# Kernel optimization log

Hardware: AMD Instinct MI355X
Metric: run time of the kernel (lower is better)

## Reference

```python
import jax, jax.numpy as jnp
import numpy as np

N_HEADS = 16
COS_SIM_SCALE = 8.0  # lucidrains flash_cosine_sim_attention default temperature
RMS_EPS = 1e-6
ROPE_THETA = 10000.0


def _rms_norm(t, g):
    # RMSNorm over head dim with learnable gain (QKNorm)
    return t * jax.lax.rsqrt(jnp.mean(t * t, axis=-1, keepdims=True) + RMS_EPS) * g


def _rotate_half(x):
    d = x.shape[-1]
    return jnp.concatenate([-x[..., d // 2:], x[..., : d // 2]], axis=-1)


def _image_rope_cos_sin(n, d, dtype):
    # 2D axial RoPE: first half of head dim encodes row position, second half column.
    side = int(np.sqrt(n))
    assert side * side == n, 'ImageRoPE expects a square token grid'
    n_freq = d // 4
    freqs = 1.0 / (ROPE_THETA ** (jnp.arange(n_freq, dtype=jnp.float32) / n_freq))
    pos = jnp.arange(side, dtype=jnp.float32)
    grid_h = jnp.repeat(pos, side)   # (n,) row index
    grid_w = jnp.tile(pos, side)     # (n,) col index
    ang_h = grid_h[:, None] * freqs  # (n, d//4)
    ang_w = grid_w[:, None] * freqs  # (n, d//4)
    # rotate-half convention: angles for dims [0:d//2] paired with [d//2:d]
    ang = jnp.concatenate([ang_h, ang_w], axis=-1)          # (n, d//2)
    ang = jnp.concatenate([ang, ang], axis=-1)              # (n, d)
    return jnp.cos(ang).astype(dtype), jnp.sin(ang).astype(dtype)


def setup_inputs() -> dict:
    key = jax.random.key(0)
    ks = jax.random.split(key, 6)
    b, n, dm = 8, 1024, 1024
    h = N_HEADS
    d = dm // h
    s = 1.0 / np.sqrt(dm)
    return {
        'x': jax.random.normal(ks[0], (b, n, dm), dtype=jnp.float32),
        'w_qkv': jax.random.normal(ks[1], (dm, 3 * dm), dtype=jnp.float32) * s,
        'b_qkv': jnp.zeros((3 * dm,), dtype=jnp.float32),
        'q_gain': jnp.ones((d,), dtype=jnp.float32),
        'k_gain': jnp.ones((d,), dtype=jnp.float32),
        'w_out': jax.random.normal(ks[2], (dm, dm), dtype=jnp.float32) * s,
        'b_out': jnp.zeros((dm,), dtype=jnp.float32),
    }


def reference(x, w_qkv, b_qkv, q_gain, k_gain, w_out, b_out):
    b, n, dm = x.shape
    h = N_HEADS
    d = dm // h
    qkv = x @ w_qkv + b_qkv                       # (b, n, 3*dm)
    qkv = qkv.reshape(b, n, 3, h, d)
    qkv = jnp.transpose(qkv, (2, 0, 3, 1, 4))     # (3, b, h, n, d)
    q, k, v = qkv[0], qkv[1], qkv[2]
    # QK-norm (RMSNorm over head dim)
    q = _rms_norm(q, q_gain)
    k = _rms_norm(k, k_gain)
    # 2D image RoPE
    cos, sin = _image_rope_cos_sin(n, d, x.dtype)
    q = q * cos + _rotate_half(q) * sin
    k = k * cos + _rotate_half(k) * sin
    # cosine-sim attention: l2-normalize q,k, fixed scale, softmax, weighted sum
    q = q / jnp.linalg.norm(q, axis=-1, keepdims=True)
    k = k / jnp.linalg.norm(k, axis=-1, keepdims=True)
    scores = jnp.einsum('bhnd,bhmd->bhnm', q, k) * COS_SIM_SCALE
    attn = jax.nn.softmax(scores, axis=-1)
    o = jnp.einsum('bhnm,bhmd->bhnd', attn, v)    # (b, h, n, d)
    o = jnp.transpose(o, (0, 2, 1, 3)).reshape(b, n, dm)
    return o @ w_out + b_out
```

## Files before the change

kernel.cpp:

```cpp
#include <hip/hip_runtime.h>
#include <hip/hip_bf16.h>
#include <cstdint>

typedef __bf16 bf16;
typedef __bf16 bf16x8 __attribute__((ext_vector_type(8)));
typedef __bf16 bf16x4 __attribute__((ext_vector_type(4)));
typedef float f32x4 __attribute__((ext_vector_type(4)));

__device__ inline bf16x8 cvt8(const float* __restrict__ p) {
  float4 a = *(const float4*)p;
  float4 b = *(const float4*)(p + 4);
  bf16x8 r;
  r[0] = (bf16)a.x; r[1] = (bf16)a.y; r[2] = (bf16)a.z; r[3] = (bf16)a.w;
  r[4] = (bf16)b.x; r[5] = (bf16)b.y; r[6] = (bf16)b.z; r[7] = (bf16)b.w;
  return r;
}

__device__ inline void gl_lds16(const bf16* g, bf16* l) {
  auto gp = reinterpret_cast<const __attribute__((address_space(1))) uint32_t*>(
      reinterpret_cast<uintptr_t>(g));
  auto lp = reinterpret_cast<__attribute__((address_space(3))) uint32_t*>(
      reinterpret_cast<uintptr_t>(l));
  __builtin_amdgcn_global_load_lds(gp, lp, 16, 0, 0);
}

#define BAR() asm volatile("s_barrier" ::: "memory")

__global__ __launch_bounds__(256) void cast_k(const float* __restrict__ in,
                                              bf16* __restrict__ out) {
  long i = ((long)blockIdx.x * 256 + threadIdx.x) * 8;
  *(bf16x8*)(out + i) = cvt8(in + i);
}

__global__ __launch_bounds__(256) void transpose_cast_k(const float* __restrict__ in,
                                                        bf16* __restrict__ out,
                                                        int R, int C) {
  __shared__ bf16 T[32][33];
  int tc = blockIdx.x * 32, tr = blockIdx.y * 32;
  int c = threadIdx.x & 31, r8 = threadIdx.x >> 5;
#pragma unroll
  for (int i = 0; i < 4; i++) {
    int r = r8 + i * 8;
    T[r][c] = (bf16)in[(long)(tr + r) * C + tc + c];
  }
  __syncthreads();
#pragma unroll
  for (int i = 0; i < 4; i++) {
    int r = r8 + i * 8;
    out[(long)(tc + r) * R + tr + c] = T[c][r];
  }
}

__global__ __launch_bounds__(512, 4) void gemm256(const bf16* __restrict__ A,
                                                  const bf16* __restrict__ Bt,
                                                  const float* __restrict__ bias,
                                                  int K,
                                                  bf16* __restrict__ qb,
                                                  bf16* __restrict__ kb,
                                                  bf16* __restrict__ v4,
                                                  const float* __restrict__ qg,
                                                  const float* __restrict__ kg) {
  __shared__ __align__(16) bf16 As[2][4096];
  __shared__ __align__(16) bf16 Bs[2][8192];

  const int tid = threadIdx.x;
  const int lane = tid & 63;
  const int w = tid >> 6;
  const int quad = lane >> 4;
  const int l16 = lane & 15;
  const int wr = w >> 2;
  const int wc = w & 3;

  const int gx = gridDim.x;
  const int bid = blockIdx.y * gx + blockIdx.x;
  const int cpx = (gx * gridDim.y) >> 3;
  const int sw = (bid & 7) * cpx + (bid >> 3);
  const int n0 = (sw % gx) * 256;
  const int m0 = (sw / gx) * 128;

  const int srA = tid >> 2;
  const int scS = ((tid & 3) ^ ((tid >> 3) & 3)) * 8;
  const bf16* aS = A + (long)(m0 + srA) * K + scS;
  const bf16* bS0 = Bt + (long)(n0 + srA) * K + scS;
  const bf16* bS1 = bS0 + (long)128 * K;

#define STAGE(tb, kt1)                                                   \
  {                                                                      \
    const long kc = (long)(kt1)*32;                                      \
    gl_lds16(aS + kc, &As[tb][w * 512]);                                 \
    gl_lds16(bS0 + kc, &Bs[tb][w * 512]);                                \
    gl_lds16(bS1 + kc, &Bs[tb][4096 + w * 512]);                         \
  }

  const int cphys = (quad ^ ((l16 >> 1) & 3)) * 8;
  const int aoff = (wr * 64 + l16) * 32 + cphys;
  const int boff = (wc * 64 + l16) * 32 + cphys;

  f32x4 acc[4][4];
#pragma unroll
  for (int i = 0; i < 4; i++)
#pragma unroll
    for (int j = 0; j < 4; j++) acc[i][j] = f32x4{0.f, 0.f, 0.f, 0.f};

  const int NK = K >> 5;
  STAGE(0, 0);

  for (int kt = 0; kt < NK; ++kt) {
    const int pb = kt & 1;
    const int tb = pb ^ 1;
    const bool pf = (kt + 1 < NK);
    if (pf) {
      STAGE(tb, kt + 1);
      asm volatile("s_waitcnt vmcnt(3)" ::: "memory");
    } else {
      asm volatile("s_waitcnt vmcnt(0)" ::: "memory");
    }
    BAR();
    bf16x8 afr[4], bfr[4];
#pragma unroll
    for (int n = 0; n < 4; n++) bfr[n] = *(const bf16x8*)&Bs[pb][boff + n * 512];
#pragma unroll
    for (int m = 0; m < 4; m++) afr[m] = *(const bf16x8*)&As[pb][aoff + m * 512];
    __builtin_amdgcn_s_setprio(1);
#pragma unroll
    for (int m = 0; m < 4; m++)
#pragma unroll
      for (int n = 0; n < 4; n++)
        acc[m][n] = __builtin_amdgcn_mfma_f32_16x16x32_bf16(afr[m], bfr[n], acc[m][n], 0, 0, 0);
    __builtin_amdgcn_s_setprio(0);
    BAR();
  }

  const int which = n0 >> 10;
  if (which == 2) {
    const int T0 = (((m0 & 1023) + wr * 64) >> 2) + quad;
    const int bh = (m0 >> 10) * 16 + (((n0 + wc * 64) & 1023) >> 6);
#pragma unroll
    for (int m = 0; m < 4; m++) {
#pragma unroll
      for (int n = 0; n < 4; n++) {
        int ng = n0 + wc * 64 + n * 16 + l16;
        int dc = n * 16 + l16;
        float bj = bias[ng];
        bf16x4 pv;
#pragma unroll
        for (int r = 0; r < 4; r++) pv[r] = (bf16)(acc[m][n][r] + bj);
        *(bf16x4*)(v4 + ((long)bh * 16384 + (long)(T0 + m * 4) * 64 + dc) * 4) = pv;
      }
    }
    return;
  }

  const float* gg = which ? kg : qg;
  bf16* dst = which ? kb : qb;
  const float fold = which ? 1.0f : 8.0f;
  const int h = ((n0 + wc * 64) & 1023) >> 6;
  const int bh = (m0 >> 10) * 16 + h;
  float bj[4], gain[4];
#pragma unroll
  for (int j = 0; j < 4; j++) {
    bj[j] = bias[n0 + wc * 64 + j * 16 + l16];
    gain[j] = gg[j * 16 + l16];
  }
  const float f = exp2f((float)l16 * (-13.287712379549449f / 16.0f));

#pragma unroll
  for (int m = 0; m < 4; m++) {
#pragma unroll
    for (int r = 0; r < 4; r++) {
      int ntok = (m0 & 1023) + wr * 64 + m * 16 + quad * 4 + r;
      float v0 = acc[m][0][r] + bj[0];
      float v1 = acc[m][1][r] + bj[1];
      float v2 = acc[m][2][r] + bj[2];
      float v3 = acc[m][3][r] + bj[3];
      float ss = v0 * v0 + v1 * v1 + v2 * v2 + v3 * v3;
#pragma unroll
      for (int mk = 1; mk <= 8; mk <<= 1) ss += __shfl_xor(ss, mk, 64);
      float rms = rsqrtf(ss * (1.0f / 64.0f) + 1e-6f);
      v0 *= rms * gain[0]; v1 *= rms * gain[1]; v2 *= rms * gain[2]; v3 *= rms * gain[3];
      float sh, ch_, swv, cw;
      __sincosf((float)(ntok >> 5) * f, &sh, &ch_);
      __sincosf((float)(ntok & 31) * f, &swv, &cw);
      float w0 = v0 * ch_ - v2 * sh;
      float w1 = v1 * cw - v3 * swv;
      float w2 = v2 * ch_ + v0 * sh;
      float w3 = v3 * cw + v1 * swv;
      float nn = w0 * w0 + w1 * w1 + w2 * w2 + w3 * w3;
#pragma unroll
      for (int mk = 1; mk <= 8; mk <<= 1) nn += __shfl_xor(nn, mk, 64);
      float inv = rsqrtf(nn) * fold;
      long base = ((long)bh * 1024 + ntok) * 64 + l16;
      dst[base] = (bf16)(w0 * inv);
      dst[base + 16] = (bf16)(w1 * inv);
      dst[base + 32] = (bf16)(w2 * inv);
      dst[base + 48] = (bf16)(w3 * inv);
    }
  }
}

__global__ __launch_bounds__(256, 5) void gemm_bt1(const bf16* __restrict__ A,
                                                   const bf16* __restrict__ Bt,
                                                   const float* __restrict__ bias,
                                                   int N, int K,
                                                   float* __restrict__ out) {
  __shared__ __align__(16) bf16 As[128][32];
  __shared__ __align__(16) bf16 Bs[128][32];

  const int tid = threadIdx.x;
  const int lane = tid & 63;
  const int w = tid >> 6;
  const int wm = (w & 1) * 64;
  const int wn = (w >> 1) * 64;
  const int quad = lane >> 4;
  const int l16 = lane & 15;

  const int m0 = blockIdx.y * 128;
  const int n0 = blockIdx.x * 128;

  const int sr = w * 32 + (lane >> 2);
  const int sc = (lane & 3) * 8;

  f32x4 acc[4][4];
#pragma unroll
  for (int i = 0; i < 4; i++)
#pragma unroll
    for (int j = 0; j < 4; j++) acc[i][j] = f32x4{0.f, 0.f, 0.f, 0.f};

  for (int k0 = 0; k0 < K; k0 += 32) {
    __syncthreads();
    int hh = k0 >> 6, dc = (k0 & 63) + sc;
    int m1 = m0 + sr, m2 = m1 + 16;
    const bf16* ga0 = A + ((long)((m1 >> 10) * 16 + hh) * 1024 + (m1 & 1023)) * 64 + dc;
    const bf16* ga1 = A + ((long)((m2 >> 10) * 16 + hh) * 1024 + (m2 & 1023)) * 64 + dc;
    gl_lds16(ga0, &As[w * 32][0]);
    gl_lds16(ga1, &As[w * 32 + 16][0]);
    gl_lds16(Bt + (long)(n0 + sr) * K + k0 + sc, &Bs[w * 32][0]);
    gl_lds16(Bt + (long)(n0 + sr + 16) * K + k0 + sc, &Bs[w * 32 + 16][0]);
    __syncthreads();

    bf16x8 af[4], bfr[4];
#pragma unroll
    for (int i = 0; i < 4; i++) {
      af[i] = *(const bf16x8*)&As[wm + i * 16 + l16][quad * 8];
      bfr[i] = *(const bf16x8*)&Bs[wn + i * 16 + l16][quad * 8];
    }
#pragma unroll
    for (int i = 0; i < 4; i++)
#pragma unroll
      for (int j = 0; j < 4; j++)
        acc[i][j] = __builtin_amdgcn_mfma_f32_16x16x32_bf16(af[i], bfr[j], acc[i][j], 0, 0, 0);
  }

#pragma unroll
  for (int i = 0; i < 4; i++)
#pragma unroll
    for (int j = 0; j < 4; j++)
#pragma unroll
      for (int r = 0; r < 4; r++) {
        int mg = m0 + wm + i * 16 + quad * 4 + r;
        int ng = n0 + wn + j * 16 + l16;
        out[(long)mg * N + ng] = acc[i][j][r] + bias[ng];
      }
}

__global__ __launch_bounds__(256, 2) void attn_k(bf16* __restrict__ qb,
                                                 const bf16* __restrict__ kb,
                                                 const bf16* __restrict__ v4) {
  __shared__ __align__(16) bf16 Ks[2][64][72];
  __shared__ __align__(16) bf16 Vl[2][4096];
  __shared__ __align__(16) bf16 Ps[4][16][72];

  const int tid = threadIdx.x;
  const int lane = tid & 63;
  const int w = tid >> 6;
  const int quad = lane >> 4;
  const int l16 = lane & 15;

  const int bh = blockIdx.y;
  const int q0 = blockIdx.x * 256 + w * 64;

  bf16x8 aq[4][2];
  long qrow[4];
#pragma unroll
  for (int g = 0; g < 4; g++) {
    qrow[g] = ((long)bh * 1024 + q0 + g * 16 + l16) * 64;
    aq[g][0] = *(const bf16x8*)(qb + qrow[g] + quad * 8);
    aq[g][1] = *(const bf16x8*)(qb + qrow[g] + 32 + quad * 8);
  }

  f32x4 o[4][4];
#pragma unroll
  for (int g = 0; g < 4; g++)
#pragma unroll
    for (int i = 0; i < 4; i++) o[g][i] = f32x4{0.f, 0.f, 0.f, 0.f};
  float ls[4] = {0.f, 0.f, 0.f, 0.f};

  const int sr = tid >> 3, sc = (tid & 7) * 8;
  const bf16* kbase = kb + (long)bh * 65536;
  const bf16* vbase = v4 + (long)bh * 65536;

  bf16x8 kr0 = *(const bf16x8*)(kbase + (long)sr * 64 + sc);
  bf16x8 kr1 = *(const bf16x8*)(kbase + (long)(sr + 32) * 64 + sc);
  gl_lds16(vbase + (w * 2) * 512 + lane * 8, &Vl[0][(w * 2) * 512]);
  gl_lds16(vbase + (w * 2 + 1) * 512 + lane * 8, &Vl[0][(w * 2 + 1) * 512]);
  asm volatile("s_waitcnt vmcnt(0)" ::: "memory");
  *(bf16x8*)&Ks[0][sr][sc] = kr0;
  *(bf16x8*)&Ks[0][sr + 32][sc] = kr1;
  asm volatile("s_waitcnt lgkmcnt(0)" ::: "memory");
  BAR();

  for (int kt = 0; kt < 1024; kt += 64) {
    const int cur = (kt >> 6) & 1;
    const bool pf = (kt + 64 < 1024);
    if (pf) {
      kr0 = *(const bf16x8*)(kbase + (long)(kt + 64 + sr) * 64 + sc);
      kr1 = *(const bf16x8*)(kbase + (long)(kt + 64 + sr + 32) * 64 + sc);
      gl_lds16(vbase + (long)(kt + 64) * 64 + (w * 2) * 512 + lane * 8,
               &Vl[cur ^ 1][(w * 2) * 512]);
      gl_lds16(vbase + (long)(kt + 64) * 64 + (w * 2 + 1) * 512 + lane * 8,
               &Vl[cur ^ 1][(w * 2 + 1) * 512]);
    }

    bf16x8 kf[4][2], vf[4][2];
#pragma unroll
    for (int i = 0; i < 4; i++) {
      kf[i][0] = *(const bf16x8*)&Ks[cur][i * 16 + l16][quad * 8];
      kf[i][1] = *(const bf16x8*)&Ks[cur][i * 16 + l16][32 + quad * 8];
      int D4 = (i * 16 + l16) * 4;
      bf16x4 a0 = *(const bf16x4*)&Vl[cur][quad * 512 + D4];
      bf16x4 a1 = *(const bf16x4*)&Vl[cur][quad * 512 + D4 + 256];
      bf16x4 a2 = *(const bf16x4*)&Vl[cur][quad * 512 + D4 + 2048];
      bf16x4 a3 = *(const bf16x4*)&Vl[cur][quad * 512 + D4 + 2048 + 256];
      vf[i][0] = __builtin_shufflevector(a0, a1, 0, 1, 2, 3, 4, 5, 6, 7);
      vf[i][1] = __builtin_shufflevector(a2, a3, 0, 1, 2, 3, 4, 5, 6, 7);
    }

#pragma unroll
    for (int g = 0; g < 4; g++) {
#pragma unroll
      for (int i = 0; i < 4; i++) {
        f32x4 st = f32x4{0.f, 0.f, 0.f, 0.f};
        st = __builtin_amdgcn_mfma_f32_16x16x32_bf16(kf[i][0], aq[g][0], st, 0, 0, 0);
        st = __builtin_amdgcn_mfma_f32_16x16x32_bf16(kf[i][1], aq[g][1], st, 0, 0, 0);
        bf16x4 pk;
#pragma unroll
        for (int r = 0; r < 4; r++) {
          float p = __expf(st[r] - 8.0f);
          ls[g] += p;
          pk[r] = (bf16)p;
        }
        *(bf16x4*)&Ps[w][l16][i * 16 + quad * 4] = pk;
      }
      asm volatile("s_waitcnt lgkmcnt(0)" ::: "memory");
      bf16x8 bp0 = *(const bf16x8*)&Ps[w][l16][quad * 8];
      bf16x8 bp1 = *(const bf16x8*)&Ps[w][l16][32 + quad * 8];
#pragma unroll
      for (int i = 0; i < 4; i++) {
        o[g][i] = __builtin_amdgcn_mfma_f32_16x16x32_bf16(vf[i][0], bp0, o[g][i], 0, 0, 0);
        o[g][i] = __builtin_amdgcn_mfma_f32_16x16x32_bf16(vf[i][1], bp1, o[g][i], 0, 0, 0);
      }
    }

    if (pf) {
      asm volatile("s_waitcnt vmcnt(0)" ::: "memory");
      *(bf16x8*)&Ks[cur ^ 1][sr][sc] = kr0;
      *(bf16x8*)&Ks[cur ^ 1][sr + 32][sc] = kr1;
    }
    asm volatile("s_waitcnt lgkmcnt(0)" ::: "memory");
    BAR();
  }

#pragma unroll
  for (int g = 0; g < 4; g++) {
    float l = ls[g];
    l += __shfl_xor(l, 16, 64);
    l += __shfl_xor(l, 32, 64);
    float inv = 1.0f / l;
#pragma unroll
    for (int i = 0; i < 4; i++) {
      bf16x4 ov;
#pragma unroll
      for (int r = 0; r < 4; r++) ov[r] = (bf16)(o[g][i][r] * inv);
      *(bf16x4*)(qb + qrow[g] + i * 16 + quad * 4) = ov;
    }
  }
}

extern "C" void kernel_launch(void* const* d_in, const int* in_sizes, int n_in,
                              void* d_out, int out_size, void* d_ws, size_t ws_size,
                              hipStream_t stream) {
  (void)in_sizes; (void)n_in; (void)out_size; (void)ws_size;
  const float* x     = (const float*)d_in[0];
  const float* w_qkv = (const float*)d_in[1];
  const float* b_qkv = (const float*)d_in[2];
  const float* q_g   = (const float*)d_in[3];
  const float* k_g   = (const float*)d_in[4];
  const float* w_out = (const float*)d_in[5];
  const float* b_out = (const float*)d_in[6];
  float* out = (float*)d_out;

  char* ws = (char*)d_ws;
  bf16* wqkvT = (bf16*)ws; ws += (long)3072 * 1024 * 2;
  bf16* woT   = (bf16*)ws; ws += (long)1024 * 1024 * 2;
  bf16* xb    = (bf16*)ws; ws += (long)8192 * 1024 * 2;
  bf16* qb    = (bf16*)ws; ws += (long)128 * 1024 * 64 * 2;
  bf16* kb    = (bf16*)ws; ws += (long)128 * 1024 * 64 * 2;
  bf16* v4    = (bf16*)ws; ws += (long)128 * 64 * 1024 * 2;

  cast_k<<<4096, 256, 0, stream>>>(x, xb);
  transpose_cast_k<<<dim3(3072 / 32, 1024 / 32), 256, 0, stream>>>(w_qkv, wqkvT, 1024, 3072);
  transpose_cast_k<<<dim3(1024 / 32, 1024 / 32), 256, 0, stream>>>(w_out, woT, 1024, 1024);
  gemm256<<<dim3(3072 / 256, 8192 / 128), 512, 0, stream>>>(xb, wqkvT, b_qkv, 1024,
                                                            qb, kb, v4, q_g, k_g);
  attn_k<<<dim3(4, 128), 256, 0, stream>>>(qb, kb, v4);
  gemm_bt1<<<dim3(1024 / 128, 8192 / 128), 256, 0, stream>>>(qb, woT, b_out,
                                                             1024, 1024, out);
}
```

Measured before the change: 261.7 us.

## Merge prep kernels, double-buffer output GEMM, software-pipeline attention PV step

Three prep kernels (x cast and two weight transpose-casts) are merged into one launch to cut launch overhead. The output-projection GEMM gets double-buffered, XOR-swizzled LDS staging with async prefetch of the next K tile and raised wave priority around the MFMAs, to hide global-load latency and reduce bank conflicts. The attention kernel double-buffers the P scratch so the PV MFMAs for one query group are issued after the next group's softmax, removing an explicit LDS wait. This costs more LDS, lowers gemm_bt1 occupancy from 5 to 4 blocks, and adds barriers per K step.

```diff
diff --git a/kernel.cpp b/kernel.cpp
--- a/kernel.cpp
+++ b/kernel.cpp
@@ -26,17 +26,32 @@
 
 #define BAR() asm volatile("s_barrier" ::: "memory")
 
-__global__ __launch_bounds__(256) void cast_k(const float* __restrict__ in,
-                                              bf16* __restrict__ out) {
-  long i = ((long)blockIdx.x * 256 + threadIdx.x) * 8;
-  *(bf16x8*)(out + i) = cvt8(in + i);
-}
-
-__global__ __launch_bounds__(256) void transpose_cast_k(const float* __restrict__ in,
-                                                        bf16* __restrict__ out,
-                                                        int R, int C) {
+__global__ __launch_bounds__(256) void prep_k(const float* __restrict__ x,
+                                              bf16* __restrict__ xb,
+                                              const float* __restrict__ wqkv,
+                                              bf16* __restrict__ wqkvT,
+                                              const float* __restrict__ wo,
+                                              bf16* __restrict__ woT) {
   __shared__ bf16 T[32][33];
-  int tc = blockIdx.x * 32, tr = blockIdx.y * 32;
+  const int bid = blockIdx.x;
+  if (bid < 4096) {
+    long i = ((long)bid * 256 + threadIdx.x) * 8;
+    *(bf16x8*)(xb + i) = cvt8(x + i);
+    return;
+  }
+  const float* in;
+  bf16* out;
+  int R, C, bx, by;
+  if (bid < 7168) {
+    int t = bid - 4096;
+    in = wqkv; out = wqkvT; R = 1024; C = 3072;
+    bx = t % 96; by = t / 96;
+  } else {
+    int t = bid - 7168;
+    in = wo; out = woT; R = 1024; C = 1024;
+    bx = t % 32; by = t / 32;
+  }
+  int tc = bx * 32, tr = by * 32;
   int c = threadIdx.x & 31, r8 = threadIdx.x >> 5;
 #pragma unroll
   for (int i = 0; i < 4; i++) {
@@ -198,13 +213,13 @@
   }
 }
 
-__global__ __launch_bounds__(256, 5) void gemm_bt1(const bf16* __restrict__ A,
+__global__ __launch_bounds__(256, 4) void gemm_bt1(const bf16* __restrict__ A,
                                                    const bf16* __restrict__ Bt,
                                                    const float* __restrict__ bias,
                                                    int N, int K,
                                                    float* __restrict__ out) {
-  __shared__ __align__(16) bf16 As[128][32];
-  __shared__ __align__(16) bf16 Bs[128][32];
+  __shared__ __align__(16) bf16 As[2][4096];
+  __shared__ __align__(16) bf16 Bs[2][4096];
 
   const int tid = threadIdx.x;
   const int lane = tid & 63;
@@ -217,8 +232,27 @@
   const int m0 = blockIdx.y * 128;
   const int n0 = blockIdx.x * 128;
 
-  const int sr = w * 32 + (lane >> 2);
-  const int sc = (lane & 3) * 8;
+  int srow[2], scof[2];
+#pragma unroll
+  for (int l = 0; l < 2; l++) {
+    int s = l * 256 + tid;
+    srow[l] = s >> 2;
+    scof[l] = ((s & 3) ^ ((s >> 3) & 3)) * 8;
+  }
+
+  auto stage = [&](int tb, int k0) {
+    int hh = k0 >> 6;
+#pragma unroll
+    for (int l = 0; l < 2; l++) {
+      int m1 = m0 + srow[l];
+      int dc = (k0 & 63) + scof[l];
+      const bf16* ga = A + ((long)((m1 >> 10) * 16 + hh) * 1024 + (m1 & 1023)) * 64 + dc;
+      gl_lds16(ga, &As[tb][l * 2048 + w * 512]);
+      gl_lds16(Bt + (long)(n0 + srow[l]) * K + k0 + scof[l], &Bs[tb][l * 2048 + w * 512]);
+    }
+  };
+
+  const int cphys = (quad ^ ((l16 >> 1) & 3)) * 8;
 
   f32x4 acc[4][4];
 #pragma unroll
@@ -226,29 +260,34 @@
 #pragma unroll
     for (int j = 0; j < 4; j++) acc[i][j] = f32x4{0.f, 0.f, 0.f, 0.f};
 
-  for (int k0 = 0; k0 < K; k0 += 32) {
-    __syncthreads();
-    int hh = k0 >> 6, dc = (k0 & 63) + sc;
-    int m1 = m0 + sr, m2 = m1 + 16;
-    const bf16* ga0 = A + ((long)((m1 >> 10) * 16 + hh) * 1024 + (m1 & 1023)) * 64 + dc;
-    const bf16* ga1 = A + ((long)((m2 >> 10) * 16 + hh) * 1024 + (m2 & 1023)) * 64 + dc;
-    gl_lds16(ga0, &As[w * 32][0]);
-    gl_lds16(ga1, &As[w * 32 + 16][0]);
-    gl_lds16(Bt + (long)(n0 + sr) * K + k0 + sc, &Bs[w * 32][0]);
-    gl_lds16(Bt + (long)(n0 + sr + 16) * K + k0 + sc, &Bs[w * 32 + 16][0]);
-    __syncthreads();
-
+  const int NK = K >> 5;
+  stage(0, 0);
+
+  for (int kt = 0; kt < NK; ++kt) {
+    const int pb = kt & 1;
+    const int tb = pb ^ 1;
+    const bool pf = (kt + 1 < NK);
+    if (pf) {
+      stage(tb, (kt + 1) << 5);
+      asm volatile("s_waitcnt vmcnt(4)" ::: "memory");
+    } else {
+      asm volatile("s_waitcnt vmcnt(0)" ::: "memory");
+    }
+    BAR();
     bf16x8 af[4], bfr[4];
 #pragma unroll
     for (int i = 0; i < 4; i++) {
-      af[i] = *(const bf16x8*)&As[wm + i * 16 + l16][quad * 8];
-      bfr[i] = *(const bf16x8*)&Bs[wn + i * 16 + l16][quad * 8];
-    }
+      af[i] = *(const bf16x8*)&As[pb][(wm + i * 16 + l16) * 32 + cphys];
+      bfr[i] = *(const bf16x8*)&Bs[pb][(wn + i * 16 + l16) * 32 + cphys];
+    }
+    __builtin_amdgcn_s_setprio(1);
 #pragma unroll
     for (int i = 0; i < 4; i++)
 #pragma unroll
       for (int j = 0; j < 4; j++)
         acc[i][j] = __builtin_amdgcn_mfma_f32_16x16x32_bf16(af[i], bfr[j], acc[i][j], 0, 0, 0);
+    __builtin_amdgcn_s_setprio(0);
+    BAR();
   }
 
 #pragma unroll
@@ -268,7 +307,7 @@
                                                  const bf16* __restrict__ v4) {
   __shared__ __align__(16) bf16 Ks[2][64][72];
   __shared__ __align__(16) bf16 Vl[2][4096];
-  __shared__ __align__(16) bf16 Ps[4][16][72];
+  __shared__ __align__(16) bf16 Ps[4][2][16][72];
 
   const int tid = threadIdx.x;
   const int lane = tid & 63;
@@ -335,8 +374,10 @@
       vf[i][1] = __builtin_shufflevector(a2, a3, 0, 1, 2, 3, 4, 5, 6, 7);
     }
 
+    bf16x8 bp[2][2];
 #pragma unroll
     for (int g = 0; g < 4; g++) {
+      const int sl = g & 1;
 #pragma unroll
       for (int i = 0; i < 4; i++) {
         f32x4 st = f32x4{0.f, 0.f, 0.f, 0.f};
@@ -349,16 +390,23 @@
           ls[g] += p;
           pk[r] = (bf16)p;
         }
-        *(bf16x4*)&Ps[w][l16][i * 16 + quad * 4] = pk;
+        *(bf16x4*)&Ps[w][sl][l16][i * 16 + quad * 4] = pk;
       }
-      asm volatile("s_waitcnt lgkmcnt(0)" ::: "memory");
-      bf16x8 bp0 = *(const bf16x8*)&Ps[w][l16][quad * 8];
-      bf16x8 bp1 = *(const bf16x8*)&Ps[w][l16][32 + quad * 8];
-#pragma unroll
-      for (int i = 0; i < 4; i++) {
-        o[g][i] = __builtin_amdgcn_mfma_f32_16x16x32_bf16(vf[i][0], bp0, o[g][i], 0, 0, 0);
-        o[g][i] = __builtin_amdgcn_mfma_f32_16x16x32_bf16(vf[i][1], bp1, o[g][i], 0, 0, 0);
+      bp[sl][0] = *(const bf16x8*)&Ps[w][sl][l16][quad * 8];
+      bp[sl][1] = *(const bf16x8*)&Ps[w][sl][l16][32 + quad * 8];
+      if (g > 0) {
+        const int pg = (g - 1) & 1;
+#pragma unroll
+        for (int i = 0; i < 4; i++) {
+          o[g - 1][i] = __builtin_amdgcn_mfma_f32_16x16x32_bf16(vf[i][0], bp[pg][0], o[g - 1][i], 0, 0, 0);
+          o[g - 1][i] = __builtin_amdgcn_mfma_f32_16x16x32_bf16(vf[i][1], bp[pg][1], o[g - 1][i], 0, 0, 0);
+        }
       }
+    }
+#pragma unroll
+    for (int i = 0; i < 4; i++) {
+      o[3][i] = __builtin_amdgcn_mfma_f32_16x16x32_bf16(vf[i][0], bp[1][0], o[3][i], 0, 0, 0);
+      o[3][i] = __builtin_amdgcn_mfma_f32_16x16x32_bf16(vf[i][1], bp[1][1], o[3][i], 0, 0, 0);
     }
 
     if (pf) {
@@ -407,9 +455,7 @@
   bf16* kb    = (bf16*)ws; ws += (long)128 * 1024 * 64 * 2;
   bf16* v4    = (bf16*)ws; ws += (long)128 * 64 * 1024 * 2;
 
-  cast_k<<<4096, 256, 0, stream>>>(x, xb);
-  transpose_cast_k<<<dim3(3072 / 32, 1024 / 32), 256, 0, stream>>>(w_qkv, wqkvT, 1024, 3072);
-  transpose_cast_k<<<dim3(1024 / 32, 1024 / 32), 256, 0, stream>>>(w_out, woT, 1024, 1024);
+  prep_k<<<8192, 256, 0, stream>>>(x, xb, w_qkv, wqkvT, w_out, woT);
   gemm256<<<dim3(3072 / 256, 8192 / 128), 512, 0, stream>>>(xb, wqkvT, b_qkv, 1024,
                                                             qb, kb, v4, q_g, k_g);
   attn_k<<<dim3(4, 128), 256, 0, stream>>>(qb, kb, v4);
```

New measurement: 246.0 us. 6.0% less time.
